# Performance work log

Measured on AMD Instinct MI355X. Metric: run time of the kernel, lower is better.

## Reference

```python
import jax, jax.numpy as jnp
import numpy as np

B, C, L, D = 8, 16, 256, 512
DIM_HEAD = 64
SCALE = DIM_HEAD ** -0.5


def setup_inputs() -> dict:
    key = jax.random.key(0)
    ks = jax.random.split(key, 9)
    s = 0.05  # small init scale to keep activations sane
    return {
        "x": jax.random.normal(ks[0], (B, C, L, D), jnp.float32),
        "w_qkv": jax.random.normal(ks[1], (D, 3 * D), jnp.float32) * s,
        "pos_emb": jax.random.normal(ks[2], (1, C, L, L), jnp.float32),
        "w1": jax.random.normal(ks[3], (L, L), jnp.float32) * s,
        "b1": jnp.zeros((L,), jnp.float32),
        "w2": jax.random.normal(ks[4], (L, 1), jnp.float32) * s,
        "b2": jnp.zeros((1,), jnp.float32),
        "w_out": jax.random.normal(ks[5], (D, D), jnp.float32) * s,
        "b_out": jnp.zeros((D,), jnp.float32),
    }


def reference(x, w_qkv, pos_emb, w1, b1, w2, b2, w_out, b_out):
    # squared index distance |j - i|^2, shape [1,1,L,L]
    idx = jnp.arange(L, dtype=x.dtype)
    dist = ((idx[None, :] - idx[:, None]) ** 2)[None, None]

    qkv = jnp.einsum('bcld,de->bcle', x, w_qkv)  # [B,C,L,3D]
    q, k, v = jnp.split(qkv, 3, axis=-1)

    dots = jnp.einsum('bcld,bcmd->bclm', q, k) * SCALE  # [B,C,L,L]
    attn = jax.nn.softmax(dots, axis=-1)

    # per-row adaptive variance via small MLP over the score row
    attn_weight = attn + pos_emb                         # [B,C,L,L]
    h = jax.nn.relu(attn_weight @ w1 + b1)               # [B,C,L,L]
    w = h @ w2 + b2                                      # [B,C,L,1]

    # Gaussian distance decay, then second softmax
    weight = jnp.exp(-dist / (2.0 * w * w + 1e-6))       # [B,C,L,L]
    attn2 = jax.nn.softmax(attn * weight, axis=-1)

    out = jnp.einsum('bclm,bcmd->bcld', attn2, v)        # [B,C,L,D]
    return out @ w_out + b_out
```

## Files before the change

kernel.cpp:

```cpp
#include <hip/hip_runtime.h>
#include <hip/hip_bf16.h>

typedef unsigned short u16;
typedef unsigned int u32;

typedef short bf16x8 __attribute__((ext_vector_type(8)));
typedef float f32x4 __attribute__((ext_vector_type(4)));

__device__ __forceinline__ u16 f2bf(float f) {
    union { float f; u32 u; } v; v.f = f;
    u32 u = v.u;
    return (u16)((u + 0x7fffu + ((u >> 16) & 1u)) >> 16);
}
__device__ __forceinline__ float bf2f(u16 b) {
    union { u32 u; float f; } v; v.u = ((u32)b) << 16;
    return v.f;
}

__device__ __forceinline__ void gload16(const u16* g, u16* lds_uniform_base, int lane) {
#if __has_builtin(__builtin_amdgcn_global_load_lds)
    __builtin_amdgcn_global_load_lds((const __attribute__((address_space(1))) void*)g,
                                     (__attribute__((address_space(3))) void*)lds_uniform_base,
                                     16, 0, 0);
#else
    *(int4*)(lds_uniform_base + lane * 8) = *(const int4*)g;
#endif
}

template<int AMODE, bool OUT_F32, bool RELU, bool HAS_BIAS>
__global__ __launch_bounds__(256) void gemm2_k(
    const u16* __restrict__ A, const u16* __restrict__ B, void* __restrict__ Cp,
    const float* __restrict__ bias, const float* __restrict__ pos, float scale,
    int K, int lda, int ldb, int ldc, long sA, long sB, long sC)
{
    __shared__ u16 As[128 * 32];
    __shared__ u16 Bs[128 * 32];

    const int tid   = threadIdx.x;
    const int lane  = tid & 63;
    const int wave  = tid >> 6;
    const int wbase = tid & ~63;
    const int wm = (wave >> 1) * 64, wn = (wave & 1) * 64;
    const int row0 = blockIdx.x * 128;
    const int col0 = blockIdx.y * 128;
    const long batch = blockIdx.z;

    const u16* Ab = A + batch * sA;
    const u16* Bb = B + batch * sB;
    const float* posb = (AMODE == 1) ? pos + (size_t)(batch & 15) * 65536 : nullptr;

    const int slotp = (lane >> 4) ^ (lane & 3) ^ ((lane >> 2) & 3);

    f32x4 acc[4][4] = {};

    for (int k0 = 0; k0 < K; k0 += 32) {
        if constexpr (AMODE == 0) {
            #pragma unroll
            for (int i = 0; i < 2; ++i) {
                int idx = tid + i * 256;
                int r = idx >> 2, c = idx & 3;
                int s = c ^ (r & 3) ^ ((r >> 2) & 3);
                gload16(Ab + (size_t)(row0 + r) * lda + k0 + s * 8,
                        &As[(size_t)(wbase + i * 256) * 8], lane);
            }
        } else {
            #pragma unroll
            for (int i = 0; i < 2; ++i) {
                int idx = tid + i * 256;
                int r = idx >> 2, c = idx & 3;
                int gr = row0 + r;
                const u16*  ap = Ab + (size_t)gr * lda + k0 + c * 8;
                const float* pp = posb + (size_t)gr * 256 + k0 + c * 8;
                int4 av4 = *(const int4*)ap;
                float4 p0 = *(const float4*)pp, p1 = *(const float4*)(pp + 4);
                const u16* ae = (const u16*)&av4;
                u16 o[8];
                o[0] = f2bf(bf2f(ae[0]) + p0.x); o[1] = f2bf(bf2f(ae[1]) + p0.y);
                o[2] = f2bf(bf2f(ae[2]) + p0.z); o[3] = f2bf(bf2f(ae[3]) + p0.w);
                o[4] = f2bf(bf2f(ae[4]) + p1.x); o[5] = f2bf(bf2f(ae[5]) + p1.y);
                o[6] = f2bf(bf2f(ae[6]) + p1.z); o[7] = f2bf(bf2f(ae[7]) + p1.w);
                int sl = c ^ (r & 3) ^ ((r >> 2) & 3);
                *(int4*)&As[(size_t)r * 32 + sl * 8] = *(const int4*)o;
            }
        }
        #pragma unroll
        for (int i = 0; i < 2; ++i) {
            int idx = tid + i * 256;
            int r = idx >> 2, c = idx & 3;
            int s = c ^ (r & 3) ^ ((r >> 2) & 3);
            gload16(Bb + (size_t)(col0 + r) * ldb + k0 + s * 8,
                    &Bs[(size_t)(wbase + i * 256) * 8], lane);
        }
        __syncthreads();

        bf16x8 a[4], b[4];
        #pragma unroll
        for (int m = 0; m < 4; ++m)
            a[m] = *(const bf16x8*)&As[(size_t)(wm + m * 16 + (lane & 15)) * 32 + slotp * 8];
        #pragma unroll
        for (int n = 0; n < 4; ++n)
            b[n] = *(const bf16x8*)&Bs[(size_t)(wn + n * 16 + (lane & 15)) * 32 + slotp * 8];
        #pragma unroll
        for (int m = 0; m < 4; ++m)
            #pragma unroll
            for (int n = 0; n < 4; ++n)
                acc[m][n] = __builtin_amdgcn_mfma_f32_16x16x32_bf16(a[m], b[n], acc[m][n], 0, 0, 0);
        __syncthreads();
    }

    float* Cf = (float*)Cp + batch * sC;
    u16*   Cb = (u16*)Cp + batch * sC;
    #pragma unroll
    for (int m = 0; m < 4; ++m) {
        #pragma unroll
        for (int n = 0; n < 4; ++n) {
            #pragma unroll
            for (int r = 0; r < 4; ++r) {
                int row = row0 + wm + m * 16 + (lane >> 4) * 4 + r;
                int col = col0 + wn + n * 16 + (lane & 15);
                float v = acc[m][n][r] * scale;
                if constexpr (HAS_BIAS) v += bias[col];
                if constexpr (RELU) v = fmaxf(v, 0.f);
                if constexpr (OUT_F32) Cf[(size_t)row * ldc + col] = v;
                else                   Cb[(size_t)row * ldc + col] = f2bf(v);
            }
        }
    }
}

__global__ __launch_bounds__(256) void trans_f2b_k(
    const float* __restrict__ in, u16* __restrict__ out, int R, int C)
{
    __shared__ u16 t[64][80];
    const int bx = blockIdx.x, by = blockIdx.y;
    const int tid = threadIdx.x;
    const int r = tid >> 2, c16 = (tid & 3) * 16;
    const float* ip = in + (size_t)(by * 64 + r) * C + bx * 64 + c16;
    #pragma unroll
    for (int j = 0; j < 4; ++j) {
        float4 v = *(const float4*)(ip + j * 4);
        t[r][c16 + j * 4 + 0] = f2bf(v.x);
        t[r][c16 + j * 4 + 1] = f2bf(v.y);
        t[r][c16 + j * 4 + 2] = f2bf(v.z);
        t[r][c16 + j * 4 + 3] = f2bf(v.w);
    }
    __syncthreads();
    const int orow = tid >> 2, oc = (tid & 3) * 16;
    u16 o[16];
    #pragma unroll
    for (int j = 0; j < 16; ++j) o[j] = t[oc + j][orow];
    u16* op = out + (size_t)(bx * 64 + orow) * R + by * 64 + oc;
    *(int4*)op       = *(const int4*)&o[0];
    *(int4*)(op + 8) = *(const int4*)&o[8];
}

__global__ __launch_bounds__(256) void trans_b2b_k(
    const u16* __restrict__ in, u16* __restrict__ out,
    int ldin, int R, long sIn, long sOut)
{
    __shared__ u16 t[64][80];
    const int bx = blockIdx.x, by = blockIdx.y;
    const long z = blockIdx.z;
    const u16* ip = in + z * sIn;
    u16* op = out + z * sOut;
    const int tid = threadIdx.x;
    const int r = tid >> 2, c16 = (tid & 3) * 16;
    const u16* src = ip + (size_t)(by * 64 + r) * ldin + bx * 64 + c16;
    *(int4*)&t[r][c16]     = *(const int4*)src;
    *(int4*)&t[r][c16 + 8] = *(const int4*)(src + 8);
    __syncthreads();
    const int orow = tid >> 2, oc = (tid & 3) * 16;
    u16 o[16];
    #pragma unroll
    for (int j = 0; j < 16; ++j) o[j] = t[oc + j][orow];
    u16* dst = op + (size_t)(bx * 64 + orow) * R + by * 64 + oc;
    *(int4*)dst       = *(const int4*)&o[0];
    *(int4*)(dst + 8) = *(const int4*)&o[8];
}

__global__ __launch_bounds__(256) void conv_b_k(
    const float* __restrict__ in, u16* __restrict__ out, int n8)
{
    int i = blockIdx.x * 256 + threadIdx.x;
    if (i >= n8) return;
    float4 a = ((const float4*)in)[i * 2], b = ((const float4*)in)[i * 2 + 1];
    u16 o[8] = { f2bf(a.x), f2bf(a.y), f2bf(a.z), f2bf(a.w),
                 f2bf(b.x), f2bf(b.y), f2bf(b.z), f2bf(b.w) };
    ((int4*)out)[i] = *(const int4*)o;
}

__global__ __launch_bounds__(256) void softmax1_k(
    const float* __restrict__ S, u16* __restrict__ attn)
{
    const int lane = threadIdx.x & 63;
    const int row  = blockIdx.x * 4 + (threadIdx.x >> 6);
    const float* s = S + (size_t)row * 256;
    float v[4];
    #pragma unroll
    for (int i = 0; i < 4; ++i) v[i] = s[lane + i * 64];
    float mx = fmaxf(fmaxf(v[0], v[1]), fmaxf(v[2], v[3]));
    #pragma unroll
    for (int o = 32; o; o >>= 1) mx = fmaxf(mx, __shfl_xor(mx, o, 64));
    float e[4], sum = 0.f;
    #pragma unroll
    for (int i = 0; i < 4; ++i) { e[i] = __expf(v[i] - mx); sum += e[i]; }
    #pragma unroll
    for (int o = 32; o; o >>= 1) sum += __shfl_xor(sum, o, 64);
    const float inv = 1.f / sum;
    #pragma unroll
    for (int i = 0; i < 4; ++i)
        attn[(size_t)row * 256 + lane + i * 64] = f2bf(e[i] * inv);
}

__global__ __launch_bounds__(256) void wrow_k(
    const u16* __restrict__ h, const float* __restrict__ w2,
    const float* __restrict__ b2, float* __restrict__ wrow)
{
    const int lane = threadIdx.x & 63;
    const int row  = blockIdx.x * 4 + (threadIdx.x >> 6);
    const u16* hr = h + (size_t)row * 256;
    float acc = 0.f;
    #pragma unroll
    for (int i = 0; i < 4; ++i) { int col = lane + i * 64; acc += bf2f(hr[col]) * w2[col]; }
    #pragma unroll
    for (int o = 32; o; o >>= 1) acc += __shfl_xor(acc, o, 64);
    if (lane == 0) wrow[row] = acc + b2[0];
}

__global__ __launch_bounds__(256) void attn2_k(
    const u16* __restrict__ attn, const float* __restrict__ wrow, u16* __restrict__ attn2)
{
    const int lane = threadIdx.x & 63;
    const int row  = blockIdx.x * 4 + (threadIdx.x >> 6);
    const int r = row & 255;
    const float w = wrow[row];
    const float inv_den = 1.f / (2.f * w * w + 1e-6f);
    float v[4];
    #pragma unroll
    for (int i = 0; i < 4; ++i) {
        int col = lane + i * 64;
        float d = (float)(col - r);
        v[i] = bf2f(attn[(size_t)row * 256 + col]) * __expf(-(d * d) * inv_den);
    }
    float mx = fmaxf(fmaxf(v[0], v[1]), fmaxf(v[2], v[3]));
    #pragma unroll
    for (int o = 32; o; o >>= 1) mx = fmaxf(mx, __shfl_xor(mx, o, 64));
    float e[4], sum = 0.f;
    #pragma unroll
    for (int i = 0; i < 4; ++i) { e[i] = __expf(v[i] - mx); sum += e[i]; }
    #pragma unroll
    for (int o = 32; o; o >>= 1) sum += __shfl_xor(sum, o, 64);
    const float inv = 1.f / sum;
    #pragma unroll
    for (int i = 0; i < 4; ++i)
        attn2[(size_t)row * 256 + lane + i * 64] = f2bf(e[i] * inv);
}

extern "C" void kernel_launch(void* const* d_in, const int* in_sizes, int n_in,
                              void* d_out, int out_size, void* d_ws, size_t ws_size,
                              hipStream_t stream) {
    const float* x     = (const float*)d_in[0];
    const float* w_qkv = (const float*)d_in[1];
    const float* pos   = (const float*)d_in[2];
    const float* w1    = (const float*)d_in[3];
    const float* b1    = (const float*)d_in[4];
    const float* w2    = (const float*)d_in[5];
    const float* b2    = (const float*)d_in[6];
    const float* w_out = (const float*)d_in[7];
    const float* b_out = (const float*)d_in[8];
    float* out = (float*)d_out;
    char* ws = (char*)d_ws;

    u16*   xb    = (u16*)(ws);
    u16*   vT    = (u16*)(ws);
    u16*   qb    = (u16*)(ws + 33554432);
    u16*   hbuf  = (u16*)(ws + 33554432);
    u16*   attn2 = (u16*)(ws + 50331648);
    u16*   kb    = (u16*)(ws + 67108864);
    u16*   attn  = (u16*)(ws + 67108864);
    u16*   vb    = (u16*)(ws + 100663296);
    float* S     = (float*)(ws + 100663296);
    u16*   av    = (u16*)(ws + 100663296);
    float* wrow  = (float*)(ws + 134217728);
    u16*   wqkvT = (u16*)(ws + 134348800);
    u16*   w1T   = (u16*)(ws + 135921664);
    u16*   woT   = (u16*)(ws + 136052736);
    if (ws_size < (size_t)136577024) return;

    dim3 blk(256);

    conv_b_k<<<dim3(8192), blk, 0, stream>>>(x, xb, 2097152);
    trans_f2b_k<<<dim3(24, 8), blk, 0, stream>>>(w_qkv, wqkvT, 512, 1536);
    trans_f2b_k<<<dim3(4, 4), blk, 0, stream>>>(w1, w1T, 256, 256);
    trans_f2b_k<<<dim3(8, 8), blk, 0, stream>>>(w_out, woT, 512, 512);

    gemm2_k<0, false, false, false><<<dim3(256, 4, 1), blk, 0, stream>>>(
        xb, wqkvT,          qb, nullptr, nullptr, 1.f, 512, 512, 512, 512, 0, 0, 0);
    gemm2_k<0, false, false, false><<<dim3(256, 4, 1), blk, 0, stream>>>(
        xb, wqkvT + 262144, kb, nullptr, nullptr, 1.f, 512, 512, 512, 512, 0, 0, 0);
    gemm2_k<0, false, false, false><<<dim3(256, 4, 1), blk, 0, stream>>>(
        xb, wqkvT + 524288, vb, nullptr, nullptr, 1.f, 512, 512, 512, 512, 0, 0, 0);

    trans_b2b_k<<<dim3(8, 4, 128), blk, 0, stream>>>(vb, vT, 512, 256, 131072L, 131072L);

    gemm2_k<0, true, false, false><<<dim3(2, 2, 128), blk, 0, stream>>>(
        qb, kb, S, nullptr, nullptr, 0.125f, 512, 512, 512, 256, 131072L, 131072L, 65536L);

    softmax1_k<<<dim3(8192), blk, 0, stream>>>(S, attn);

    gemm2_k<1, false, true, true><<<dim3(2, 2, 128), blk, 0, stream>>>(
        attn, w1T, hbuf, b1, pos, 1.f, 256, 256, 256, 256, 65536L, 0L, 65536L);

    wrow_k<<<dim3(8192), blk, 0, stream>>>(hbuf, w2, b2, wrow);

    attn2_k<<<dim3(8192), blk, 0, stream>>>(attn, wrow, attn2);

    gemm2_k<0, false, false, false><<<dim3(2, 4, 128), blk, 0, stream>>>(
        attn2, vT, av, nullptr, nullptr, 1.f, 256, 256, 256, 512, 65536L, 131072L, 131072L);

    gemm2_k<0, true, false, true><<<dim3(256, 4, 1), blk, 0, stream>>>(
        av, woT, out, b_out, nullptr, 1.f, 512, 512, 512, 512, 0, 0, 0);
}
```

Before: 380.9 us.

## Fuse attention, MLP, second softmax, AV and output projection into one kernel

Replaces the QK^T GEMM, both softmaxes, the per-row MLP, the Gaussian decay, the AV GEMM and the output projection with one kernel, `fused_k`. Each 512-thread block owns 128 query rows of one (b,c) slice. The intermediates (attn + pos, attn2, av) stay in a 128KB swizzled LDS buffer, and the w2 reduction is done from registers instead of going through HBM. The three QKV projection GEMMs are also merged into one launch using the batch grid dimension. This removes large fp32/bf16 intermediate round-trips and many kernel launches. The cost is a serial chain of GEMMs inside each block, no global-to-LDS double buffering, and roughly one block per CU because of the LDS footprint.

Result: faster. 337.7 us (-11.3%).

```diff
diff --git a/kernel.cpp b/kernel.cpp
--- a/kernel.cpp
+++ b/kernel.cpp
@@ -39,7 +39,6 @@
     const int tid   = threadIdx.x;
     const int lane  = tid & 63;
     const int wave  = tid >> 6;
-    const int wbase = tid & ~63;
     const int wm = (wave >> 1) * 64, wn = (wave & 1) * 64;
     const int row0 = blockIdx.x * 128;
     const int col0 = blockIdx.y * 128;
@@ -47,41 +46,19 @@
 
     const u16* Ab = A + batch * sA;
     const u16* Bb = B + batch * sB;
-    const float* posb = (AMODE == 1) ? pos + (size_t)(batch & 15) * 65536 : nullptr;
 
     const int slotp = (lane >> 4) ^ (lane & 3) ^ ((lane >> 2) & 3);
 
     f32x4 acc[4][4] = {};
 
     for (int k0 = 0; k0 < K; k0 += 32) {
-        if constexpr (AMODE == 0) {
-            #pragma unroll
-            for (int i = 0; i < 2; ++i) {
-                int idx = tid + i * 256;
-                int r = idx >> 2, c = idx & 3;
-                int s = c ^ (r & 3) ^ ((r >> 2) & 3);
-                gload16(Ab + (size_t)(row0 + r) * lda + k0 + s * 8,
-                        &As[(size_t)(wbase + i * 256) * 8], lane);
-            }
-        } else {
-            #pragma unroll
-            for (int i = 0; i < 2; ++i) {
-                int idx = tid + i * 256;
-                int r = idx >> 2, c = idx & 3;
-                int gr = row0 + r;
-                const u16*  ap = Ab + (size_t)gr * lda + k0 + c * 8;
-                const float* pp = posb + (size_t)gr * 256 + k0 + c * 8;
-                int4 av4 = *(const int4*)ap;
-                float4 p0 = *(const float4*)pp, p1 = *(const float4*)(pp + 4);
-                const u16* ae = (const u16*)&av4;
-                u16 o[8];
-                o[0] = f2bf(bf2f(ae[0]) + p0.x); o[1] = f2bf(bf2f(ae[1]) + p0.y);
-                o[2] = f2bf(bf2f(ae[2]) + p0.z); o[3] = f2bf(bf2f(ae[3]) + p0.w);
-                o[4] = f2bf(bf2f(ae[4]) + p1.x); o[5] = f2bf(bf2f(ae[5]) + p1.y);
-                o[6] = f2bf(bf2f(ae[6]) + p1.z); o[7] = f2bf(bf2f(ae[7]) + p1.w);
-                int sl = c ^ (r & 3) ^ ((r >> 2) & 3);
-                *(int4*)&As[(size_t)r * 32 + sl * 8] = *(const int4*)o;
-            }
+        #pragma unroll
+        for (int i = 0; i < 2; ++i) {
+            int idx = tid + i * 256;
+            int r = idx >> 2, c = idx & 3;
+            int s = c ^ (r & 3) ^ ((r >> 2) & 3);
+            gload16(Ab + (size_t)(row0 + r) * lda + k0 + s * 8,
+                    &As[(idx & ~63) * 8], lane);
         }
         #pragma unroll
         for (int i = 0; i < 2; ++i) {
@@ -89,17 +66,17 @@
             int r = idx >> 2, c = idx & 3;
             int s = c ^ (r & 3) ^ ((r >> 2) & 3);
             gload16(Bb + (size_t)(col0 + r) * ldb + k0 + s * 8,
-                    &Bs[(size_t)(wbase + i * 256) * 8], lane);
+                    &Bs[(idx & ~63) * 8], lane);
         }
         __syncthreads();
 
         bf16x8 a[4], b[4];
         #pragma unroll
         for (int m = 0; m < 4; ++m)
-            a[m] = *(const bf16x8*)&As[(size_t)(wm + m * 16 + (lane & 15)) * 32 + slotp * 8];
+            a[m] = *(const bf16x8*)&As[(wm + m * 16 + (lane & 15)) * 32 + slotp * 8];
         #pragma unroll
         for (int n = 0; n < 4; ++n)
-            b[n] = *(const bf16x8*)&Bs[(size_t)(wn + n * 16 + (lane & 15)) * 32 + slotp * 8];
+            b[n] = *(const bf16x8*)&Bs[(wn + n * 16 + (lane & 15)) * 32 + slotp * 8];
         #pragma unroll
         for (int m = 0; m < 4; ++m)
             #pragma unroll
@@ -116,7 +93,7 @@
         for (int n = 0; n < 4; ++n) {
             #pragma unroll
             for (int r = 0; r < 4; ++r) {
-                int row = row0 + wm + m * 16 + (lane >> 4) * 4 + r;
+                int row = row0 + wm + m * 16 + ((lane >> 4)) * 4 + r;
                 int col = col0 + wn + n * 16 + (lane & 15);
                 float v = acc[m][n][r] * scale;
                 if constexpr (HAS_BIAS) v += bias[col];
@@ -128,6 +105,288 @@
     }
 }
 
+__device__ __forceinline__ void stage_b256(const u16* __restrict__ src, int ld, int k0,
+                                           u16* Bs, int tid, int lane) {
+    #pragma unroll
+    for (int i = 0; i < 2; ++i) {
+        int idx = tid + i * 512;
+        int r = idx >> 2, c = idx & 3;
+        int s = c ^ (r & 3) ^ ((r >> 2) & 3);
+        gload16(src + (size_t)r * ld + k0 + s * 8, &Bs[(idx & ~63) * 8], lane);
+    }
+}
+
+__device__ __forceinline__ bf16x8 rdW(const u16* W, int row, int chunk) {
+    return *(const bf16x8*)&W[row * 512 + (chunk ^ (row & 7)) * 8];
+}
+__device__ __forceinline__ void wrW(u16* W, int row, int col, u16 v) {
+    W[row * 512 + (((col >> 3) ^ (row & 7)) * 8) + (col & 7)] = v;
+}
+
+__device__ __forceinline__ void gemm_from_W(
+    f32x4 (&dst)[4][4], const u16* __restrict__ Bsrc, int ldb, int K, int cbase,
+    const u16* W, u16* Bs, int tid, int lane, int wm, int wn, int l15, int l4, int slotp)
+{
+    #pragma unroll
+    for (int m = 0; m < 4; ++m)
+        #pragma unroll
+        for (int n = 0; n < 4; ++n) dst[m][n] = f32x4{0.f, 0.f, 0.f, 0.f};
+    for (int k0 = 0; k0 < K; k0 += 32) {
+        stage_b256(Bsrc, ldb, k0, Bs, tid, lane);
+        __syncthreads();
+        bf16x8 a[4], b[4];
+        #pragma unroll
+        for (int m = 0; m < 4; ++m)
+            a[m] = rdW(W, wm + m * 16 + l15, cbase + (k0 >> 3) + l4);
+        #pragma unroll
+        for (int n = 0; n < 4; ++n)
+            b[n] = *(const bf16x8*)&Bs[(wn + n * 16 + l15) * 32 + slotp * 8];
+        #pragma unroll
+        for (int m = 0; m < 4; ++m)
+            #pragma unroll
+            for (int n = 0; n < 4; ++n)
+                dst[m][n] = __builtin_amdgcn_mfma_f32_16x16x32_bf16(a[m], b[n], dst[m][n], 0, 0, 0);
+        __syncthreads();
+    }
+}
+
+__device__ __forceinline__ void row_softmax(
+    f32x4 (&val)[4][4], float (&red)[128][4], int wm, int wnidx, int l15, int l4)
+{
+    float rm[4][4];
+    #pragma unroll
+    for (int m = 0; m < 4; ++m)
+        #pragma unroll
+        for (int rr = 0; rr < 4; ++rr) {
+            float x = fmaxf(fmaxf(val[m][0][rr], val[m][1][rr]),
+                            fmaxf(val[m][2][rr], val[m][3][rr]));
+            #pragma unroll
+            for (int o = 1; o < 16; o <<= 1) x = fmaxf(x, __shfl_xor(x, o, 64));
+            rm[m][rr] = x;
+        }
+    if (l15 == 0)
+        #pragma unroll
+        for (int m = 0; m < 4; ++m)
+            #pragma unroll
+            for (int rr = 0; rr < 4; ++rr)
+                red[wm + m * 16 + l4 * 4 + rr][wnidx] = rm[m][rr];
+    __syncthreads();
+    #pragma unroll
+    for (int m = 0; m < 4; ++m)
+        #pragma unroll
+        for (int rr = 0; rr < 4; ++rr) {
+            float4 rv = *(const float4*)&red[wm + m * 16 + l4 * 4 + rr][0];
+            rm[m][rr] = fmaxf(fmaxf(rv.x, rv.y), fmaxf(rv.z, rv.w));
+        }
+    __syncthreads();
+    float rs[4][4];
+    #pragma unroll
+    for (int m = 0; m < 4; ++m)
+        #pragma unroll
+        for (int rr = 0; rr < 4; ++rr) {
+            float s = 0.f;
+            #pragma unroll
+            for (int n = 0; n < 4; ++n) {
+                float e = __expf(val[m][n][rr] - rm[m][rr]);
+                val[m][n][rr] = e;
+                s += e;
+            }
+            #pragma unroll
+            for (int o = 1; o < 16; o <<= 1) s += __shfl_xor(s, o, 64);
+            rs[m][rr] = s;
+        }
+    if (l15 == 0)
+        #pragma unroll
+        for (int m = 0; m < 4; ++m)
+            #pragma unroll
+            for (int rr = 0; rr < 4; ++rr)
+                red[wm + m * 16 + l4 * 4 + rr][wnidx] = rs[m][rr];
+    __syncthreads();
+    #pragma unroll
+    for (int m = 0; m < 4; ++m)
+        #pragma unroll
+        for (int rr = 0; rr < 4; ++rr) {
+            float4 rv = *(const float4*)&red[wm + m * 16 + l4 * 4 + rr][0];
+            float inv = 1.f / (rv.x + rv.y + rv.z + rv.w);
+            #pragma unroll
+            for (int n = 0; n < 4; ++n) val[m][n][rr] *= inv;
+        }
+    __syncthreads();
+}
+
+__global__ __launch_bounds__(512, 2) void fused_k(
+    const u16* __restrict__ qb, const u16* __restrict__ kb, const u16* __restrict__ vT,
+    const u16* __restrict__ w1T, const u16* __restrict__ woT,
+    const float* __restrict__ pos, const float* __restrict__ b1v,
+    const float* __restrict__ w2v, const float* __restrict__ b2v,
+    const float* __restrict__ bov, float* __restrict__ out)
+{
+    __shared__ u16 As[128 * 32];
+    __shared__ u16 Bs[256 * 32];
+    __shared__ u16 W[128 * 512];
+    __shared__ float red[128][4];
+    __shared__ float wr[128];
+
+    const int tid  = threadIdx.x;
+    const int lane = tid & 63;
+    const int wid  = tid >> 6;
+    const int wm = (wid >> 2) * 64;
+    const int wn = (wid & 3) * 64;
+    const int l15 = lane & 15, l4 = lane >> 4;
+    const int slotp = l4 ^ (lane & 3) ^ ((lane >> 2) & 3);
+    const int row0 = blockIdx.x * 128;
+    const int z    = blockIdx.y;
+
+    const u16* q = qb + (size_t)z * 131072 + (size_t)row0 * 512;
+    const u16* k = kb + (size_t)z * 131072;
+    const u16* v = vT + (size_t)z * 131072;
+    const float* posb = pos + (size_t)(z & 15) * 65536 + (size_t)row0 * 256;
+    const float b2s = b2v[0];
+
+    f32x4 sa[4][4] = {};
+    f32x4 acc[4][4] = {};
+
+    for (int k0 = 0; k0 < 512; k0 += 32) {
+        {
+            int r = tid >> 2, c = tid & 3;
+            int s = c ^ (r & 3) ^ ((r >> 2) & 3);
+            gload16(q + (size_t)r * 512 + k0 + s * 8, &As[(tid & ~63) * 8], lane);
+        }
+        stage_b256(k, 512, k0, Bs, tid, lane);
+        __syncthreads();
+        bf16x8 a[4], b[4];
+        #pragma unroll
+        for (int m = 0; m < 4; ++m)
+            a[m] = *(const bf16x8*)&As[(wm + m * 16 + l15) * 32 + slotp * 8];
+        #pragma unroll
+        for (int n = 0; n < 4; ++n)
+            b[n] = *(const bf16x8*)&Bs[(wn + n * 16 + l15) * 32 + slotp * 8];
+        #pragma unroll
+        for (int m = 0; m < 4; ++m)
+            #pragma unroll
+            for (int n = 0; n < 4; ++n)
+                sa[m][n] = __builtin_amdgcn_mfma_f32_16x16x32_bf16(a[m], b[n], sa[m][n], 0, 0, 0);
+        __syncthreads();
+    }
+
+    #pragma unroll
+    for (int m = 0; m < 4; ++m)
+        #pragma unroll
+        for (int n = 0; n < 4; ++n) sa[m][n] *= 0.125f;
+    row_softmax(sa, red, wm, wid & 3, l15, l4);
+    #pragma unroll
+    for (int m = 0; m < 4; ++m)
+        #pragma unroll
+        for (int rr = 0; rr < 4; ++rr) {
+            int row = wm + m * 16 + l4 * 4 + rr;
+            #pragma unroll
+            for (int n = 0; n < 4; ++n) {
+                int col = wn + n * 16 + l15;
+                wrW(W, row, col, f2bf(sa[m][n][rr] + posb[row * 256 + col]));
+            }
+        }
+
+    float b1c[4], w2c[4];
+    #pragma unroll
+    for (int n = 0; n < 4; ++n) {
+        int col = wn + n * 16 + l15;
+        b1c[n] = b1v[col];
+        w2c[n] = w2v[col];
+    }
+    gemm_from_W(acc, w1T, 256, 256, 0, W, Bs, tid, lane, wm, wn, l15, l4, slotp);
+    {
+        float part[4][4];
+        #pragma unroll
+        for (int m = 0; m < 4; ++m)
+            #pragma unroll
+            for (int rr = 0; rr < 4; ++rr) {
+                float p = 0.f;
+                #pragma unroll
+                for (int n = 0; n < 4; ++n)
+                    p += fmaxf(acc[m][n][rr] + b1c[n], 0.f) * w2c[n];
+                #pragma unroll
+                for (int o = 1; o < 16; o <<= 1) p += __shfl_xor(p, o, 64);
+                part[m][rr] = p;
+            }
+        if (l15 == 0)
+            #pragma unroll
+            for (int m = 0; m < 4; ++m)
+                #pragma unroll
+                for (int rr = 0; rr < 4; ++rr)
+                    red[wm + m * 16 + l4 * 4 + rr][wid & 3] = part[m][rr];
+        __syncthreads();
+        if ((wid & 3) == 0 && l15 == 0)
+            #pragma unroll
+            for (int m = 0; m < 4; ++m)
+                #pragma unroll
+                for (int rr = 0; rr < 4; ++rr) {
+                    int row = wm + m * 16 + l4 * 4 + rr;
+                    float4 rv = *(const float4*)&red[row][0];
+                    wr[row] = rv.x + rv.y + rv.z + rv.w + b2s;
+                }
+        __syncthreads();
+    }
+
+    #pragma unroll
+    for (int m = 0; m < 4; ++m)
+        #pragma unroll
+        for (int rr = 0; rr < 4; ++rr) {
+            int row = wm + m * 16 + l4 * 4 + rr;
+            float wv = wr[row];
+            float idn = 1.f / (2.f * wv * wv + 1e-6f);
+            int rg = row0 + row;
+            #pragma unroll
+            for (int n = 0; n < 4; ++n) {
+                float d = (float)(wn + n * 16 + l15 - rg);
+                sa[m][n][rr] *= __expf(-d * d * idn);
+            }
+        }
+    row_softmax(sa, red, wm, wid & 3, l15, l4);
+    #pragma unroll
+    for (int m = 0; m < 4; ++m)
+        #pragma unroll
+        for (int rr = 0; rr < 4; ++rr) {
+            int row = wm + m * 16 + l4 * 4 + rr;
+            #pragma unroll
+            for (int n = 0; n < 4; ++n)
+                wrW(W, row, 256 + wn + n * 16 + l15, f2bf(sa[m][n][rr]));
+        }
+
+    gemm_from_W(sa,  v,                  256, 256, 32, W, Bs, tid, lane, wm, wn, l15, l4, slotp);
+    gemm_from_W(acc, v + 256 * 256,      256, 256, 32, W, Bs, tid, lane, wm, wn, l15, l4, slotp);
+
+    #pragma unroll
+    for (int m = 0; m < 4; ++m)
+        #pragma unroll
+        for (int rr = 0; rr < 4; ++rr) {
+            int row = wm + m * 16 + l4 * 4 + rr;
+            #pragma unroll
+            for (int n = 0; n < 4; ++n) {
+                int col = wn + n * 16 + l15;
+                wrW(W, row, col,       f2bf(sa[m][n][rr]));
+                wrW(W, row, col + 256, f2bf(acc[m][n][rr]));
+            }
+        }
+
+    for (int np = 0; np < 2; ++np) {
+        gemm_from_W(acc, woT + (size_t)np * 256 * 512, 512, 512, 0,
+                    W, Bs, tid, lane, wm, wn, l15, l4, slotp);
+        float boc[4];
+        #pragma unroll
+        for (int n = 0; n < 4; ++n) boc[n] = bov[np * 256 + wn + n * 16 + l15];
+        #pragma unroll
+        for (int m = 0; m < 4; ++m)
+            #pragma unroll
+            for (int rr = 0; rr < 4; ++rr) {
+                int row = row0 + wm + m * 16 + l4 * 4 + rr;
+                size_t ob = ((size_t)z * 256 + row) * 512 + np * 256;
+                #pragma unroll
+                for (int n = 0; n < 4; ++n)
+                    out[ob + wn + n * 16 + l15] = acc[m][n][rr] + boc[n];
+            }
+    }
+}
+
 __global__ __launch_bounds__(256) void trans_f2b_k(
     const float* __restrict__ in, u16* __restrict__ out, int R, int C)
 {
@@ -138,11 +397,11 @@
     const float* ip = in + (size_t)(by * 64 + r) * C + bx * 64 + c16;
     #pragma unroll
     for (int j = 0; j < 4; ++j) {
-        float4 v = *(const float4*)(ip + j * 4);
-        t[r][c16 + j * 4 + 0] = f2bf(v.x);
-        t[r][c16 + j * 4 + 1] = f2bf(v.y);
-        t[r][c16 + j * 4 + 2] = f2bf(v.z);
-        t[r][c16 + j * 4 + 3] = f2bf(v.w);
+        float4 vv = *(const float4*)(ip + j * 4);
+        t[r][c16 + j * 4 + 0] = f2bf(vv.x);
+        t[r][c16 + j * 4 + 1] = f2bf(vv.y);
+        t[r][c16 + j * 4 + 2] = f2bf(vv.z);
+        t[r][c16 + j * 4 + 3] = f2bf(vv.w);
     }
     __syncthreads();
     const int orow = tid >> 2, oc = (tid & 3) * 16;
@@ -160,9 +419,9 @@
 {
     __shared__ u16 t[64][80];
     const int bx = blockIdx.x, by = blockIdx.y;
-    const long z = blockIdx.z;
-    const u16* ip = in + z * sIn;
-    u16* op = out + z * sOut;
+    const long zz = blockIdx.z;
+    const u16* ip = in + zz * sIn;
+    u16* op = out + zz * sOut;
     const int tid = threadIdx.x;
     const int r = tid >> 2, c16 = (tid & 3) * 16;
     const u16* src = ip + (size_t)(by * 64 + r) * ldin + bx * 64 + c16;
@@ -187,73 +446,6 @@
     u16 o[8] = { f2bf(a.x), f2bf(a.y), f2bf(a.z), f2bf(a.w),
                  f2bf(b.x), f2bf(b.y), f2bf(b.z), f2bf(b.w) };
     ((int4*)out)[i] = *(const int4*)o;
-}
-
-__global__ __launch_bounds__(256) void softmax1_k(
-    const float* __restrict__ S, u16* __restrict__ attn)
-{
-    const int lane = threadIdx.x & 63;
-    const int row  = blockIdx.x * 4 + (threadIdx.x >> 6);
-    const float* s = S + (size_t)row * 256;
-    float v[4];
-    #pragma unroll
-    for (int i = 0; i < 4; ++i) v[i] = s[lane + i * 64];
-    float mx = fmaxf(fmaxf(v[0], v[1]), fmaxf(v[2], v[3]));
-    #pragma unroll
-    for (int o = 32; o; o >>= 1) mx = fmaxf(mx, __shfl_xor(mx, o, 64));
-    float e[4], sum = 0.f;
-    #pragma unroll
-    for (int i = 0; i < 4; ++i) { e[i] = __expf(v[i] - mx); sum += e[i]; }
-    #pragma unroll
-    for (int o = 32; o; o >>= 1) sum += __shfl_xor(sum, o, 64);
-    const float inv = 1.f / sum;
-    #pragma unroll
-    for (int i = 0; i < 4; ++i)
-        attn[(size_t)row * 256 + lane + i * 64] = f2bf(e[i] * inv);
-}
-
-__global__ __launch_bounds__(256) void wrow_k(
-    const u16* __restrict__ h, const float* __restrict__ w2,
-    const float* __restrict__ b2, float* __restrict__ wrow)
-{
-    const int lane = threadIdx.x & 63;
-    const int row  = blockIdx.x * 4 + (threadIdx.x >> 6);
-    const u16* hr = h + (size_t)row * 256;
-    float acc = 0.f;
-    #pragma unroll
-    for (int i = 0; i < 4; ++i) { int col = lane + i * 64; acc += bf2f(hr[col]) * w2[col]; }
-    #pragma unroll
-    for (int o = 32; o; o >>= 1) acc += __shfl_xor(acc, o, 64);
-    if (lane == 0) wrow[row] = acc + b2[0];
-}
-
-__global__ __launch_bounds__(256) void attn2_k(
-    const u16* __restrict__ attn, const float* __restrict__ wrow, u16* __restrict__ attn2)
-{
-    const int lane = threadIdx.x & 63;
-    const int row  = blockIdx.x * 4 + (threadIdx.x >> 6);
-    const int r = row & 255;
-    const float w = wrow[row];
-    const float inv_den = 1.f / (2.f * w * w + 1e-6f);
-    float v[4];
-    #pragma unroll
-    for (int i = 0; i < 4; ++i) {
-        int col = lane + i * 64;
-        float d = (float)(col - r);
-        v[i] = bf2f(attn[(size_t)row * 256 + col]) * __expf(-(d * d) * inv_den);
-    }
-    float mx = fmaxf(fmaxf(v[0], v[1]), fmaxf(v[2], v[3]));
-    #pragma unroll
-    for (int o = 32; o; o >>= 1) mx = fmaxf(mx, __shfl_xor(mx, o, 64));
-    float e[4], sum = 0.f;
-    #pragma unroll
-    for (int i = 0; i < 4; ++i) { e[i] = __expf(v[i] - mx); sum += e[i]; }
-    #pragma unroll
-    for (int o = 32; o; o >>= 1) sum += __shfl_xor(sum, o, 64);
-    const float inv = 1.f / sum;
-    #pragma unroll
-    for (int i = 0; i < 4; ++i)
-        attn2[(size_t)row * 256 + lane + i * 64] = f2bf(e[i] * inv);
 }
 
 extern "C" void kernel_launch(void* const* d_in, const int* in_sizes, int n_in,
@@ -271,21 +463,17 @@
     float* out = (float*)d_out;
     char* ws = (char*)d_ws;
 
-    u16*   xb    = (u16*)(ws);
-    u16*   vT    = (u16*)(ws);
-    u16*   qb    = (u16*)(ws + 33554432);
-    u16*   hbuf  = (u16*)(ws + 33554432);
-    u16*   attn2 = (u16*)(ws + 50331648);
-    u16*   kb    = (u16*)(ws + 67108864);
-    u16*   attn  = (u16*)(ws + 67108864);
-    u16*   vb    = (u16*)(ws + 100663296);
-    float* S     = (float*)(ws + 100663296);
-    u16*   av    = (u16*)(ws + 100663296);
-    float* wrow  = (float*)(ws + 134217728);
-    u16*   wqkvT = (u16*)(ws + 134348800);
-    u16*   w1T   = (u16*)(ws + 135921664);
-    u16*   woT   = (u16*)(ws + 136052736);
-    if (ws_size < (size_t)136577024) return;
+    u16* xb    = (u16*)(ws);
+    u16* vT    = (u16*)(ws);
+    u16* qkvb  = (u16*)(ws + 33554432);
+    u16* wqkvT = (u16*)(ws + 134217728);
+    u16* w1T   = (u16*)(ws + 135790592);
+    u16* woT   = (u16*)(ws + 135921664);
+    if (ws_size < (size_t)136445952) return;
+
+    u16* qb = qkvb;
+    u16* kb = qkvb + 16777216;
+    u16* vb = qkvb + 33554432;
 
     dim3 blk(256);
 
@@ -294,30 +482,12 @@
     trans_f2b_k<<<dim3(4, 4), blk, 0, stream>>>(w1, w1T, 256, 256);
     trans_f2b_k<<<dim3(8, 8), blk, 0, stream>>>(w_out, woT, 512, 512);
 
-    gemm2_k<0, false, false, false><<<dim3(256, 4, 1), blk, 0, stream>>>(
-        xb, wqkvT,          qb, nullptr, nullptr, 1.f, 512, 512, 512, 512, 0, 0, 0);
-    gemm2_k<0, false, false, false><<<dim3(256, 4, 1), blk, 0, stream>>>(
-        xb, wqkvT + 262144, kb, nullptr, nullptr, 1.f, 512, 512, 512, 512, 0, 0, 0);
-    gemm2_k<0, false, false, false><<<dim3(256, 4, 1), blk, 0, stream>>>(
-        xb, wqkvT + 524288, vb, nullptr, nullptr, 1.f, 512, 512, 512, 512, 0, 0, 0);
+    gemm2_k<0, false, false, false><<<dim3(256, 4, 3), blk, 0, stream>>>(
+        xb, wqkvT, qkvb, nullptr, nullptr, 1.f, 512, 512, 512, 512,
+        0L, 262144L, 16777216L);
 
     trans_b2b_k<<<dim3(8, 4, 128), blk, 0, stream>>>(vb, vT, 512, 256, 131072L, 131072L);
 
-    gemm2_k<0, true, false, false><<<dim3(2, 2, 128), blk, 0, stream>>>(
-        qb, kb, S, nullptr, nullptr, 0.125f, 512, 512, 512, 256, 131072L, 131072L, 65536L);
-
-    softmax1_k<<<dim3(8192), blk, 0, stream>>>(S, attn);
-
-    gemm2_k<1, false, true, true><<<dim3(2, 2, 128), blk, 0, stream>>>(
-        attn, w1T, hbuf, b1, pos, 1.f, 256, 256, 256, 256, 65536L, 0L, 65536L);
-
-    wrow_k<<<dim3(8192), blk, 0, stream>>>(hbuf, w2, b2, wrow);
-
-    attn2_k<<<dim3(8192), blk, 0, stream>>>(attn, wrow, attn2);
-
-    gemm2_k<0, false, false, false><<<dim3(2, 4, 128), blk, 0, stream>>>(
-        attn2, vT, av, nullptr, nullptr, 1.f, 256, 256, 256, 512, 65536L, 131072L, 131072L);
-
-    gemm2_k<0, true, false, true><<<dim3(256, 4, 1), blk, 0, stream>>>(
-        av, woT, out, b_out, nullptr, 1.f, 512, 512, 512, 512, 0, 0, 0);
-}
+    fused_k<<<dim3(2, 128), dim3(512), 0, stream>>>(
+        qb, kb, vT, w1T, woT, pos, b1, w2, b2, b_out, out);
+}
```
